# Performance work log

Measured on AMD Instinct MI355X. Metric: run time of the kernel, lower is better.

## Reference

```python
import jax, jax.numpy as jnp
import numpy as np

N = 50000
E = 800000
IN_C = 64
OUT_C = 64
K = 2
GATE_C = IN_C + OUT_C
LAMBDA_MAX = 2.0


def _lap_norm(edge_index, edge_weight, n):
    # PyG ChebConv norm: sym Laplacian L = I - D^-1/2 A D^-1/2, scaled 2L/lmax - I.
    # With lambda_max=2 the diagonal term is (2/lmax)*1 - 1 = 0, so only the
    # off-diagonal weights -(2/lmax) * w_norm remain.
    row, col = edge_index[0], edge_index[1]
    deg = jax.ops.segment_sum(edge_weight, row, num_segments=n)
    dinv = jnp.where(deg > 0, jax.lax.rsqrt(jnp.where(deg > 0, deg, 1.0)), 0.0)
    lw = -(2.0 / LAMBDA_MAX) * edge_weight * dinv[row] * dinv[col]
    diag = jnp.full((n,), 2.0 / LAMBDA_MAX - 1.0, edge_weight.dtype)  # zeros for lmax=2
    return row, col, lw, diag


def _cheb_conv(x, row, col, lw, diag, Ws, b):
    # Ws: [K, C_in, C_out]; Tx_0 = x, Tx_1 = L_hat x, Tx_k = 2 L_hat Tx_{k-1} - Tx_{k-2}
    n = x.shape[0]

    def prop(h):  # L_hat @ h  via edge gather/scatter + diagonal
        msg = lw[:, None] * h[col]                      # [E, C]
        return jax.ops.segment_sum(msg, row, num_segments=n) + diag[:, None] * h

    Tx0 = x
    out = Tx0 @ Ws[0]
    Tx1 = prop(x)
    out = out + Tx1 @ Ws[1]
    for k in range(2, K):
        Tx2 = 2.0 * prop(Tx1) - Tx0
        out = out + Tx2 @ Ws[k]
        Tx0, Tx1 = Tx1, Tx2
    return out + b


def setup_inputs() -> dict:
    key = jax.random.key(0)
    ks = jax.random.split(key, 10)
    scale = 1.0 / np.sqrt(GATE_C)
    x = jax.random.normal(ks[0], (N, IN_C), jnp.float32)
    edge_index = jax.random.randint(ks[1], (2, E), 0, N, jnp.int64)
    edge_weight = jax.random.uniform(ks[2], (E,), jnp.float32)
    hidden_state = jax.random.normal(ks[3], (N, OUT_C), jnp.float32)
    Wz = jax.random.normal(ks[4], (K, GATE_C, OUT_C), jnp.float32) * scale
    Wr = jax.random.normal(ks[5], (K, GATE_C, OUT_C), jnp.float32) * scale
    Wh = jax.random.normal(ks[6], (K, GATE_C, OUT_C), jnp.float32) * scale
    bz = jnp.zeros((OUT_C,), jnp.float32)
    br = jnp.zeros((OUT_C,), jnp.float32)
    bh = jnp.zeros((OUT_C,), jnp.float32)
    return {"x": x, "edge_index": edge_index, "edge_weight": edge_weight,
            "hidden_state": hidden_state, "Wz": Wz, "bz": bz,
            "Wr": Wr, "br": br, "Wh": Wh, "bh": bh}


def reference(x, edge_index, edge_weight, hidden_state, Wz, bz, Wr, br, Wh, bh):
    n = x.shape[0]
    row, col, lw, diag = _lap_norm(edge_index, edge_weight, n)
    gate_input = jnp.concatenate([x, hidden_state], axis=-1)          # [N, GATE_C]
    z = jax.nn.sigmoid(_cheb_conv(gate_input, row, col, lw, diag, Wz, bz))
    r = jax.nn.sigmoid(_cheb_conv(gate_input, row, col, lw, diag, Wr, br))
    cand_in = jnp.concatenate([x, r * hidden_state], axis=-1)
    h_tilde = jnp.tanh(_cheb_conv(cand_in, row, col, lw, diag, Wh, bh))
    return (1.0 - z) * hidden_state + z * h_tilde
```

## Files before the change

kernel.cpp:

```cpp
#include <hip/hip_runtime.h>
#include <cstdint>

#define N_NODES 50000
#define N_EDGES 800000
#define C 64
#define SLOTS 64
#define B_N 120
#define NB 417
#define PCAP 2560
#define STG_BLOCKS 126
#define STG_CHUNK 6350

typedef __attribute__((ext_vector_type(8))) short bf16x8;
typedef __attribute__((ext_vector_type(4))) float f32x4;

static constexpr size_t OFF_GCUR = 0;
static constexpr size_t OFF_DINV = 512;
static constexpr size_t OFF_CNT  = 50688;
static constexpr size_t OFF_BZR  = 100864;
static constexpr size_t OFF_BH   = 117248;
static constexpr size_t OFF_CSR  = 125440;
static constexpr size_t OFF_XH   = OFF_CSR + (size_t)N_NODES * 64;
static constexpr size_t OFF_XB   = OFF_XH + (size_t)N_NODES * C;
static constexpr size_t OFF_HB   = OFF_XB + (size_t)N_NODES * C / 2;
static constexpr size_t OFF_PXB  = OFF_HB + (size_t)N_NODES * C / 2;
static constexpr size_t OFF_PHB  = OFF_PXB + (size_t)N_NODES * C / 2;
static constexpr size_t OFF_RHB  = OFF_PHB + (size_t)N_NODES * C / 2;
static constexpr size_t OFF_RHD  = OFF_RHB + (size_t)N_NODES * C / 2;
static constexpr size_t OFF_STG  = OFF_PXB;

__device__ __forceinline__ short f2bf(float f) {
    unsigned u = __float_as_uint(f);
    u += 0x7fffu + ((u >> 16) & 1u);
    return (short)(u >> 16);
}
__device__ __forceinline__ float bf_lo(unsigned v) { return __uint_as_float(v << 16); }
__device__ __forceinline__ float bf_hi(unsigned v) { return __uint_as_float(v & 0xffff0000u); }
__device__ __forceinline__ float bfu(unsigned short v) { return __uint_as_float((unsigned)v << 16); }
__device__ __forceinline__ float fast_sigmoid(float v) { return 1.f / (1.f + __expf(-v)); }
__device__ __forceinline__ float fast_tanh(float v) { return 1.f - 2.f / (__expf(2.f * v) + 1.f); }

__global__ __launch_bounds__(256) void zero_pack_kernel(
        int* __restrict__ gcur,
        const float* __restrict__ Wz, const float* __restrict__ Wr,
        const float* __restrict__ Wh,
        short* __restrict__ Bzr, short* __restrict__ Bh) {
    if (blockIdx.x == 24) {
        gcur[threadIdx.x] = 0;
        gcur[256 + threadIdx.x] = 0;
        return;
    }
    int gid = blockIdx.x * 256 + threadIdx.x;
    if (gid < 4096) {
        int ktct = gid >> 6, lane = gid & 63;
        int kt = ktct >> 3, ct = ktct & 7;
        int colg = ct * 16 + (lane & 15);
        int k0 = kt * 32 + (lane >> 4) * 8;
        const float* W = (colg < 64) ? Wz : Wr;
        int c = colg & 63;
        short v[8];
        #pragma unroll
        for (int j = 0; j < 8; ++j) {
            int k = k0 + j;
            v[j] = f2bf(W[(k >> 7) * (128 * 64) + (k & 127) * 64 + c]);
        }
        *(bf16x8*)(Bzr + (size_t)ktct * 512 + lane * 8) = *(bf16x8*)v;
    } else {
        int idx = gid - 4096;
        int ktct = idx >> 6, lane = idx & 63;
        int kt = ktct >> 2, ct = ktct & 3;
        int colg = ct * 16 + (lane & 15);
        int k0 = kt * 32 + (lane >> 4) * 8;
        short v[8];
        #pragma unroll
        for (int j = 0; j < 8; ++j) {
            int k = k0 + j;
            v[j] = f2bf(Wh[(k >> 7) * (128 * 64) + (k & 127) * 64 + colg]);
        }
        *(bf16x8*)(Bh + (size_t)ktct * 512 + lane * 8) = *(bf16x8*)v;
    }
}

__global__ __launch_bounds__(512) void stage_kernel(
        const int* __restrict__ row, const int* __restrict__ col,
        const float* __restrict__ w,
        int* __restrict__ gcur, uint2* __restrict__ stg) {
    __shared__ int lcnt[NB];
    __shared__ int lbase[NB];
    int tid = threadIdx.x;
    int e0 = blockIdx.x * STG_CHUNK;
    int e1 = min(e0 + STG_CHUNK, N_EDGES);
    for (int i = tid; i < NB; i += 512) lcnt[i] = 0;
    __syncthreads();
    for (int e = e0 + tid; e < e1; e += 512)
        atomicAdd(&lcnt[row[e] / B_N], 1);
    __syncthreads();
    for (int i = tid; i < NB; i += 512) {
        int c = lcnt[i];
        lbase[i] = c ? atomicAdd(&gcur[i], c) : 0;
        lcnt[i] = 0;
    }
    __syncthreads();
    for (int e = e0 + tid; e < e1; e += 512) {
        int r = row[e];
        int b = r / B_N;
        int off = atomicAdd(&lcnt[b], 1);
        int pos = lbase[b] + off;
        unsigned cw = ((unsigned)col[e] << 16) | (unsigned short)f2bf(w[e]);
        if (pos < PCAP)
            stg[(size_t)b * PCAP + pos] = make_uint2((unsigned)(r - b * B_N), cw);
    }
}

__global__ __launch_bounds__(256) void sort_kernel(
        const int* __restrict__ gcur, const uint2* __restrict__ stg,
        const float* __restrict__ x, const float* __restrict__ h,
        unsigned* __restrict__ csr, int* __restrict__ cnt, float* __restrict__ dinv,
        unsigned* __restrict__ xh,
        unsigned short* __restrict__ xb, unsigned short* __restrict__ hb) {
    __shared__ int lcnt[B_N];
    __shared__ int lbase[B_N];
    __shared__ float ldeg[B_N];
    __shared__ float ldv[B_N];
    __shared__ int scanb[128];
    __shared__ unsigned lbuf[PCAP];
    __shared__ unsigned char lnode[PCAP];
    int b = blockIdx.x, tid = threadIdx.x;
    int n0 = b * B_N;
    int m = min(gcur[b], PCAP);
    for (int i = tid; i < B_N; i += 256) { lcnt[i] = 0; ldeg[i] = 0.f; }
    __syncthreads();
    const uint2* s = stg + (size_t)b * PCAP;
    for (int i = tid; i < m; i += 256) {
        uint2 e = s[i];
        atomicAdd(&lcnt[e.x], 1);
        atomicAdd(&ldeg[e.x], bf_lo(e.y));
    }
    __syncthreads();
    if (tid < 128) scanb[tid] = (tid < B_N) ? lcnt[tid] : 0;
    __syncthreads();
    for (int d = 1; d < 128; d <<= 1) {
        int v = 0;
        if (tid < 128 && tid >= d) v = scanb[tid - d];
        __syncthreads();
        if (tid < 128) scanb[tid] += v;
        __syncthreads();
    }
    if (tid < B_N) { lbase[tid] = scanb[tid] - lcnt[tid]; lcnt[tid] = 0; }
    __syncthreads();
    for (int i = tid; i < m; i += 256) {
        uint2 e = s[i];
        int off = atomicAdd(&lcnt[e.x], 1);
        int p = lbase[e.x] + off;
        lbuf[p] = e.y;
        lnode[p] = (unsigned char)e.x;
    }
    __syncthreads();
    for (int i = tid; i < m; i += 256) {
        int nl = lnode[i];
        int pos = i - lbase[nl];
        csr[(size_t)(n0 + nl) * SLOTS + pos] = lbuf[i];
    }
    if (tid < B_N) {
        int node = n0 + tid;
        if (node < N_NODES) {
            cnt[node] = lcnt[tid];
            float d = ldeg[tid];
            float dv = (d > 0.f) ? rsqrtf(d) : 0.f;
            dinv[node] = dv;
            ldv[tid] = dv;
        } else ldv[tid] = 0.f;
    }
    __syncthreads();
    for (int i = tid; i < B_N * 16; i += 256) {
        int g = n0 * 16 + i;
        if (g >= N_NODES * 16) continue;
        float dv = ldv[i >> 4];
        float4 xv = ((const float4*)x)[g];
        float4 hv = ((const float4*)h)[g];
        uint4 o;
        o.x = ((unsigned)(unsigned short)f2bf(hv.x * dv) << 16) | (unsigned short)f2bf(xv.x * dv);
        o.y = ((unsigned)(unsigned short)f2bf(hv.y * dv) << 16) | (unsigned short)f2bf(xv.y * dv);
        o.z = ((unsigned)(unsigned short)f2bf(hv.z * dv) << 16) | (unsigned short)f2bf(xv.z * dv);
        o.w = ((unsigned)(unsigned short)f2bf(hv.w * dv) << 16) | (unsigned short)f2bf(xv.w * dv);
        ((uint4*)xh)[g] = o;
        ((short4*)xb)[g] = make_short4(f2bf(xv.x), f2bf(xv.y), f2bf(xv.z), f2bf(xv.w));
        ((short4*)hb)[g] = make_short4(f2bf(hv.x), f2bf(hv.y), f2bf(hv.z), f2bf(hv.w));
    }
}

__global__ __launch_bounds__(256) void prop2_gather_kernel(
        const int* __restrict__ cnt, const unsigned* __restrict__ csr,
        const float* __restrict__ dinv, const unsigned* __restrict__ xh,
        unsigned short* __restrict__ Pxb, unsigned short* __restrict__ Phb) {
    int n = (blockIdx.x * 256 + threadIdx.x) >> 6;
    int lane = threadIdx.x & 63;
    if (n >= N_NODES) return;
    int m = min(cnt[n], SLOTS);
    const unsigned* s = csr + (size_t)n * SLOTS;
    float ax = 0.f, ah = 0.f;
    int e = 0;
    for (; e + 4 <= m; e += 4) {
        unsigned p0 = s[e], p1 = s[e + 1], p2 = s[e + 2], p3 = s[e + 3];
        unsigned v0 = xh[(p0 >> 16) * C + lane];
        unsigned v1 = xh[(p1 >> 16) * C + lane];
        unsigned v2 = xh[(p2 >> 16) * C + lane];
        unsigned v3 = xh[(p3 >> 16) * C + lane];
        float w0 = bf_lo(p0), w1 = bf_lo(p1), w2 = bf_lo(p2), w3 = bf_lo(p3);
        ax = fmaf(w0, bf_lo(v0), ax);  ah = fmaf(w0, bf_hi(v0), ah);
        ax = fmaf(w1, bf_lo(v1), ax);  ah = fmaf(w1, bf_hi(v1), ah);
        ax = fmaf(w2, bf_lo(v2), ax);  ah = fmaf(w2, bf_hi(v2), ah);
        ax = fmaf(w3, bf_lo(v3), ax);  ah = fmaf(w3, bf_hi(v3), ah);
    }
    for (; e < m; ++e) {
        unsigned p = s[e];
        unsigned v = xh[(p >> 16) * C + lane];
        float wv = bf_lo(p);
        ax = fmaf(wv, bf_lo(v), ax);
        ah = fmaf(wv, bf_hi(v), ah);
    }
    float sc = -dinv[n];
    Pxb[(size_t)n * C + lane] = (unsigned short)f2bf(sc * ax);
    Phb[(size_t)n * C + lane] = (unsigned short)f2bf(sc * ah);
}

__global__ __launch_bounds__(256) void prop1_gather_kernel(
        const int* __restrict__ cnt, const unsigned* __restrict__ csr,
        const float* __restrict__ dinv,
        const unsigned short* __restrict__ rhd, unsigned short* __restrict__ Prhb) {
    int n = (blockIdx.x * 256 + threadIdx.x) >> 6;
    int lane = threadIdx.x & 63;
    if (n >= N_NODES) return;
    int m = min(cnt[n], SLOTS);
    const unsigned* s = csr + (size_t)n * SLOTS;
    float acc = 0.f;
    int e = 0;
    for (; e + 4 <= m; e += 4) {
        unsigned p0 = s[e], p1 = s[e + 1], p2 = s[e + 2], p3 = s[e + 3];
        float v0 = bfu(rhd[(p0 >> 16) * C + lane]);
        float v1 = bfu(rhd[(p1 >> 16) * C + lane]);
        float v2 = bfu(rhd[(p2 >> 16) * C + lane]);
        float v3 = bfu(rhd[(p3 >> 16) * C + lane]);
        acc = fmaf(bf_lo(p0), v0, acc);
        acc = fmaf(bf_lo(p1), v1, acc);
        acc = fmaf(bf_lo(p2), v2, acc);
        acc = fmaf(bf_lo(p3), v3, acc);
    }
    for (; e < m; ++e) {
        unsigned p = s[e];
        acc = fmaf(bf_lo(p), bfu(rhd[(p >> 16) * C + lane]), acc);
    }
    Prhb[(size_t)n * C + lane] = (unsigned short)f2bf(-dinv[n] * acc);
}

__global__ __launch_bounds__(256) void gemm_zr_mfma_kernel(
        const unsigned short* __restrict__ xb, const unsigned short* __restrict__ hb,
        const unsigned short* __restrict__ Pxb, const unsigned short* __restrict__ Phb,
        const short* __restrict__ Bzr,
        const float* __restrict__ bz, const float* __restrict__ br,
        const float* __restrict__ dinv,
        float* __restrict__ z, unsigned short* __restrict__ rhb,
        unsigned short* __restrict__ rhd) {
    int wave = (blockIdx.x * 256 + threadIdx.x) >> 6;
    int lane = threadIdx.x & 63;
    int node0 = wave * 16;
    if (node0 >= N_NODES) return;
    int q = lane >> 4;
    int nodeA = node0 + (lane & 15);

    f32x4 acc[8];
    #pragma unroll
    for (int i = 0; i < 8; ++i) acc[i] = (f32x4){0.f, 0.f, 0.f, 0.f};

    const bf16x8* Bp = (const bf16x8*)Bzr;
    #pragma unroll
    for (int kt = 0; kt < 8; ++kt) {
        const unsigned short* src = (kt < 2) ? xb : (kt < 4) ? hb : (kt < 6) ? Pxb : Phb;
        bf16x8 a = *(const bf16x8*)(src + (size_t)nodeA * C + (kt & 1) * 32 + q * 8);
        #pragma unroll
        for (int ct = 0; ct < 8; ++ct) {
            bf16x8 bfr = Bp[(kt * 8 + ct) * 64 + lane];
            acc[ct] = __builtin_amdgcn_mfma_f32_16x16x32_bf16(a, bfr, acc[ct], 0, 0, 0);
        }
    }

    float dv[4];
    #pragma unroll
    for (int r = 0; r < 4; ++r) dv[r] = dinv[node0 + q * 4 + r];

    #pragma unroll
    for (int ct = 0; ct < 8; ++ct) {
        int colg = ct * 16 + (lane & 15);
        if (ct < 4) {
            float bias = bz[colg];
            #pragma unroll
            for (int r = 0; r < 4; ++r) {
                int node = node0 + q * 4 + r;
                z[(size_t)node * C + colg] = fast_sigmoid(acc[ct][r] + bias);
            }
        } else {
            int oc = colg - 64;
            float bias = br[oc];
            #pragma unroll
            for (int r = 0; r < 4; ++r) {
                int node = node0 + q * 4 + r;
                float sg = fast_sigmoid(acc[ct][r] + bias);
                float rhv = sg * bfu(hb[(size_t)node * C + oc]);
                rhb[(size_t)node * C + oc] = (unsigned short)f2bf(rhv);
                rhd[(size_t)node * C + oc] = (unsigned short)f2bf(rhv * dv[r]);
            }
        }
    }
}

__global__ __launch_bounds__(256) void gemm_h_mfma_kernel(
        const unsigned short* __restrict__ xb, const unsigned short* __restrict__ rhb,
        const unsigned short* __restrict__ Pxb, const unsigned short* __restrict__ Prhb,
        const short* __restrict__ Bh, const float* __restrict__ bh,
        const float* __restrict__ z,  const float* __restrict__ h,
        float* __restrict__ out) {
    int wave = (blockIdx.x * 256 + threadIdx.x) >> 6;
    int lane = threadIdx.x & 63;
    int node0 = wave * 16;
    if (node0 >= N_NODES) return;
    int q = lane >> 4;
    int nodeA = node0 + (lane & 15);

    f32x4 acc[4];
    #pragma unroll
    for (int i = 0; i < 4; ++i) acc[i] = (f32x4){0.f, 0.f, 0.f, 0.f};

    const bf16x8* Bp = (const bf16x8*)Bh;
    #pragma unroll
    for (int kt = 0; kt < 8; ++kt) {
        const unsigned short* src = (kt < 2) ? xb : (kt < 4) ? rhb : (kt < 6) ? Pxb : Prhb;
        bf16x8 a = *(const bf16x8*)(src + (size_t)nodeA * C + (kt & 1) * 32 + q * 8);
        #pragma unroll
        for (int ct = 0; ct < 4; ++ct) {
            bf16x8 bfr = Bp[(kt * 4 + ct) * 64 + lane];
            acc[ct] = __builtin_amdgcn_mfma_f32_16x16x32_bf16(a, bfr, acc[ct], 0, 0, 0);
        }
    }

    #pragma unroll
    for (int ct = 0; ct < 4; ++ct) {
        int oc = ct * 16 + (lane & 15);
        float bias = bh[oc];
        #pragma unroll
        for (int r = 0; r < 4; ++r) {
            int node = node0 + q * 4 + r;
            float ht = fast_tanh(acc[ct][r] + bias);
            float zz = z[(size_t)node * C + oc];
            float hv = h[(size_t)node * C + oc];
            out[(size_t)node * C + oc] = (1.f - zz) * hv + zz * ht;
        }
    }
}

extern "C" void kernel_launch(void* const* d_in, const int* in_sizes, int n_in,
                              void* d_out, int out_size, void* d_ws, size_t ws_size,
                              hipStream_t stream) {
    const float* x    = (const float*)d_in[0];
    const int*   eidx = (const int*)  d_in[1];
    const float* w    = (const float*)d_in[2];
    const float* h    = (const float*)d_in[3];
    const float* Wz   = (const float*)d_in[4];
    const float* bz   = (const float*)d_in[5];
    const float* Wr   = (const float*)d_in[6];
    const float* br   = (const float*)d_in[7];
    const float* Wh   = (const float*)d_in[8];
    const float* bh   = (const float*)d_in[9];
    float* out = (float*)d_out;
    float* ws  = (float*)d_ws;

    const int* row = eidx;
    const int* col = eidx + N_EDGES;

    int*            gcur = (int*)(ws + OFF_GCUR);
    float*          dinv = ws + OFF_DINV;
    int*            cnt  = (int*)(ws + OFF_CNT);
    unsigned*       csr  = (unsigned*)(ws + OFF_CSR);
    short*          Bzr  = (short*)(ws + OFF_BZR);
    short*          Bh   = (short*)(ws + OFF_BH);
    unsigned*       xh   = (unsigned*)(ws + OFF_XH);
    unsigned short* xb   = (unsigned short*)(ws + OFF_XB);
    unsigned short* hb   = (unsigned short*)(ws + OFF_HB);
    unsigned short* Pxb  = (unsigned short*)(ws + OFF_PXB);
    unsigned short* Phb  = (unsigned short*)(ws + OFF_PHB);
    unsigned short* rhb  = (unsigned short*)(ws + OFF_RHB);
    unsigned short* rhd  = (unsigned short*)(ws + OFF_RHD);
    uint2*          stg  = (uint2*)(ws + OFF_STG);
    float*          z    = out;

    zero_pack_kernel<<<25, 256, 0, stream>>>(gcur, Wz, Wr, Wh, Bzr, Bh);

    stage_kernel<<<STG_BLOCKS, 512, 0, stream>>>(row, col, w, gcur, stg);

    sort_kernel<<<NB, 256, 0, stream>>>(gcur, stg, x, h, csr, cnt, dinv, xh, xb, hb);

    prop2_gather_kernel<<<(N_NODES * 64 + 255) / 256, 256, 0, stream>>>(
        cnt, csr, dinv, xh, Pxb, Phb);

    {
        int waves = (N_NODES + 15) / 16;
        int blocks = (waves + 3) / 4;
        gemm_zr_mfma_kernel<<<blocks, 256, 0, stream>>>(
            xb, hb, Pxb, Phb, Bzr, bz, br, dinv, z, rhb, rhd);
    }

    prop1_gather_kernel<<<(N_NODES * 64 + 255) / 256, 256, 0, stream>>>(
        cnt, csr, dinv, rhd, Phb);

    {
        int waves = (N_NODES + 15) / 16;
        int blocks = (waves + 3) / 4;
        gemm_h_mfma_kernel<<<blocks, 256, 0, stream>>>(
            xb, rhb, Pxb, Phb, Bh, bh, z, h, out);
    }
}
```

Before: 228.5 us.

## Fuse sparse gather propagation into MFMA gate GEMM kernels via shared memory

Merges each gather-based Laplacian propagation kernel with the MFMA GEMM that consumes it. Each 256-thread block now handles 16 nodes: its waves gather propagated rows into LDS, synchronise, then split the output column tiles among themselves. This drops two kernel launches and the global round trip of Phb/Prhb, at the cost of fewer waves per node tile during the GEMM and a block-level barrier between gather and GEMM. Pxb is still written to global memory because the h-gate kernel needs it.

```diff
diff --git a/kernel.cpp b/kernel.cpp
--- a/kernel.cpp
+++ b/kernel.cpp
@@ -189,122 +189,104 @@
     }
 }
 
-__global__ __launch_bounds__(256) void prop2_gather_kernel(
+__global__ __launch_bounds__(256) void prop_gemm_zr_kernel(
         const int* __restrict__ cnt, const unsigned* __restrict__ csr,
         const float* __restrict__ dinv, const unsigned* __restrict__ xh,
-        unsigned short* __restrict__ Pxb, unsigned short* __restrict__ Phb) {
-    int n = (blockIdx.x * 256 + threadIdx.x) >> 6;
-    int lane = threadIdx.x & 63;
-    if (n >= N_NODES) return;
-    int m = min(cnt[n], SLOTS);
-    const unsigned* s = csr + (size_t)n * SLOTS;
-    float ax = 0.f, ah = 0.f;
-    int e = 0;
-    for (; e + 4 <= m; e += 4) {
-        unsigned p0 = s[e], p1 = s[e + 1], p2 = s[e + 2], p3 = s[e + 3];
-        unsigned v0 = xh[(p0 >> 16) * C + lane];
-        unsigned v1 = xh[(p1 >> 16) * C + lane];
-        unsigned v2 = xh[(p2 >> 16) * C + lane];
-        unsigned v3 = xh[(p3 >> 16) * C + lane];
-        float w0 = bf_lo(p0), w1 = bf_lo(p1), w2 = bf_lo(p2), w3 = bf_lo(p3);
-        ax = fmaf(w0, bf_lo(v0), ax);  ah = fmaf(w0, bf_hi(v0), ah);
-        ax = fmaf(w1, bf_lo(v1), ax);  ah = fmaf(w1, bf_hi(v1), ah);
-        ax = fmaf(w2, bf_lo(v2), ax);  ah = fmaf(w2, bf_hi(v2), ah);
-        ax = fmaf(w3, bf_lo(v3), ax);  ah = fmaf(w3, bf_hi(v3), ah);
-    }
-    for (; e < m; ++e) {
-        unsigned p = s[e];
-        unsigned v = xh[(p >> 16) * C + lane];
-        float wv = bf_lo(p);
-        ax = fmaf(wv, bf_lo(v), ax);
-        ah = fmaf(wv, bf_hi(v), ah);
-    }
-    float sc = -dinv[n];
-    Pxb[(size_t)n * C + lane] = (unsigned short)f2bf(sc * ax);
-    Phb[(size_t)n * C + lane] = (unsigned short)f2bf(sc * ah);
-}
-
-__global__ __launch_bounds__(256) void prop1_gather_kernel(
-        const int* __restrict__ cnt, const unsigned* __restrict__ csr,
-        const float* __restrict__ dinv,
-        const unsigned short* __restrict__ rhd, unsigned short* __restrict__ Prhb) {
-    int n = (blockIdx.x * 256 + threadIdx.x) >> 6;
-    int lane = threadIdx.x & 63;
-    if (n >= N_NODES) return;
-    int m = min(cnt[n], SLOTS);
-    const unsigned* s = csr + (size_t)n * SLOTS;
-    float acc = 0.f;
-    int e = 0;
-    for (; e + 4 <= m; e += 4) {
-        unsigned p0 = s[e], p1 = s[e + 1], p2 = s[e + 2], p3 = s[e + 3];
-        float v0 = bfu(rhd[(p0 >> 16) * C + lane]);
-        float v1 = bfu(rhd[(p1 >> 16) * C + lane]);
-        float v2 = bfu(rhd[(p2 >> 16) * C + lane]);
-        float v3 = bfu(rhd[(p3 >> 16) * C + lane]);
-        acc = fmaf(bf_lo(p0), v0, acc);
-        acc = fmaf(bf_lo(p1), v1, acc);
-        acc = fmaf(bf_lo(p2), v2, acc);
-        acc = fmaf(bf_lo(p3), v3, acc);
-    }
-    for (; e < m; ++e) {
-        unsigned p = s[e];
-        acc = fmaf(bf_lo(p), bfu(rhd[(p >> 16) * C + lane]), acc);
-    }
-    Prhb[(size_t)n * C + lane] = (unsigned short)f2bf(-dinv[n] * acc);
-}
-
-__global__ __launch_bounds__(256) void gemm_zr_mfma_kernel(
         const unsigned short* __restrict__ xb, const unsigned short* __restrict__ hb,
-        const unsigned short* __restrict__ Pxb, const unsigned short* __restrict__ Phb,
         const short* __restrict__ Bzr,
         const float* __restrict__ bz, const float* __restrict__ br,
-        const float* __restrict__ dinv,
+        unsigned short* __restrict__ Pxb,
         float* __restrict__ z, unsigned short* __restrict__ rhb,
         unsigned short* __restrict__ rhd) {
-    int wave = (blockIdx.x * 256 + threadIdx.x) >> 6;
-    int lane = threadIdx.x & 63;
-    int node0 = wave * 16;
-    if (node0 >= N_NODES) return;
+    __shared__ __align__(16) unsigned short lpx[16][72];
+    __shared__ __align__(16) unsigned short lph[16][72];
+    int tid = threadIdx.x;
+    int wid = tid >> 6, lane = tid & 63;
+    int node0 = blockIdx.x * 16;
+
+    #pragma unroll
+    for (int i = 0; i < 4; ++i) {
+        int nl = wid * 4 + i;
+        int n = node0 + nl;
+        int m = min(cnt[n], SLOTS);
+        const unsigned* s = csr + (size_t)n * SLOTS;
+        float ax = 0.f, ah = 0.f;
+        int e = 0;
+        for (; e + 4 <= m; e += 4) {
+            unsigned p0 = s[e], p1 = s[e + 1], p2 = s[e + 2], p3 = s[e + 3];
+            unsigned v0 = xh[(p0 >> 16) * C + lane];
+            unsigned v1 = xh[(p1 >> 16) * C + lane];
+            unsigned v2 = xh[(p2 >> 16) * C + lane];
+            unsigned v3 = xh[(p3 >> 16) * C + lane];
+            float w0 = bf_lo(p0), w1 = bf_lo(p1), w2 = bf_lo(p2), w3 = bf_lo(p3);
+            ax = fmaf(w0, bf_lo(v0), ax);  ah = fmaf(w0, bf_hi(v0), ah);
+            ax = fmaf(w1, bf_lo(v1), ax);  ah = fmaf(w1, bf_hi(v1), ah);
+            ax = fmaf(w2, bf_lo(v2), ax);  ah = fmaf(w2, bf_hi(v2), ah);
+            ax = fmaf(w3, bf_lo(v3), ax);  ah = fmaf(w3, bf_hi(v3), ah);
+        }
+        for (; e < m; ++e) {
+            unsigned p = s[e];
+            unsigned v = xh[(p >> 16) * C + lane];
+            float wv = bf_lo(p);
+            ax = fmaf(wv, bf_lo(v), ax);
+            ah = fmaf(wv, bf_hi(v), ah);
+        }
+        float sc = -dinv[n];
+        unsigned short px = (unsigned short)f2bf(sc * ax);
+        unsigned short ph = (unsigned short)f2bf(sc * ah);
+        lpx[nl][lane] = px;
+        lph[nl][lane] = ph;
+        Pxb[(size_t)n * C + lane] = px;
+    }
+    __syncthreads();
+
     int q = lane >> 4;
-    int nodeA = node0 + (lane & 15);
-
-    f32x4 acc[8];
-    #pragma unroll
-    for (int i = 0; i < 8; ++i) acc[i] = (f32x4){0.f, 0.f, 0.f, 0.f};
-
+    int nl = lane & 15;
+    f32x4 acc[2];
+    acc[0] = (f32x4){0.f, 0.f, 0.f, 0.f};
+    acc[1] = (f32x4){0.f, 0.f, 0.f, 0.f};
     const bf16x8* Bp = (const bf16x8*)Bzr;
     #pragma unroll
     for (int kt = 0; kt < 8; ++kt) {
-        const unsigned short* src = (kt < 2) ? xb : (kt < 4) ? hb : (kt < 6) ? Pxb : Phb;
-        bf16x8 a = *(const bf16x8*)(src + (size_t)nodeA * C + (kt & 1) * 32 + q * 8);
-        #pragma unroll
-        for (int ct = 0; ct < 8; ++ct) {
+        bf16x8 a;
+        if (kt < 4) {
+            const unsigned short* src = (kt < 2) ? xb : hb;
+            a = *(const bf16x8*)(src + (size_t)(node0 + nl) * C + (kt & 1) * 32 + q * 8);
+        } else {
+            const unsigned short* src = (kt < 6) ? &lpx[0][0] : &lph[0][0];
+            a = *(const bf16x8*)(src + nl * 72 + (kt & 1) * 32 + q * 8);
+        }
+        #pragma unroll
+        for (int c2 = 0; c2 < 2; ++c2) {
+            int ct = wid * 2 + c2;
             bf16x8 bfr = Bp[(kt * 8 + ct) * 64 + lane];
-            acc[ct] = __builtin_amdgcn_mfma_f32_16x16x32_bf16(a, bfr, acc[ct], 0, 0, 0);
-        }
-    }
-
-    float dv[4];
-    #pragma unroll
-    for (int r = 0; r < 4; ++r) dv[r] = dinv[node0 + q * 4 + r];
-
-    #pragma unroll
-    for (int ct = 0; ct < 8; ++ct) {
-        int colg = ct * 16 + (lane & 15);
-        if (ct < 4) {
+            acc[c2] = __builtin_amdgcn_mfma_f32_16x16x32_bf16(a, bfr, acc[c2], 0, 0, 0);
+        }
+    }
+
+    if (wid < 2) {
+        #pragma unroll
+        for (int c2 = 0; c2 < 2; ++c2) {
+            int colg = (wid * 2 + c2) * 16 + nl;
             float bias = bz[colg];
             #pragma unroll
             for (int r = 0; r < 4; ++r) {
                 int node = node0 + q * 4 + r;
-                z[(size_t)node * C + colg] = fast_sigmoid(acc[ct][r] + bias);
+                z[(size_t)node * C + colg] = fast_sigmoid(acc[c2][r] + bias);
             }
-        } else {
-            int oc = colg - 64;
+        }
+    } else {
+        float dv[4];
+        #pragma unroll
+        for (int r = 0; r < 4; ++r) dv[r] = dinv[node0 + q * 4 + r];
+        #pragma unroll
+        for (int c2 = 0; c2 < 2; ++c2) {
+            int oc = (wid * 2 + c2 - 4) * 16 + nl;
             float bias = br[oc];
             #pragma unroll
             for (int r = 0; r < 4; ++r) {
                 int node = node0 + q * 4 + r;
-                float sg = fast_sigmoid(acc[ct][r] + bias);
+                float sg = fast_sigmoid(acc[c2][r] + bias);
                 float rhv = sg * bfu(hb[(size_t)node * C + oc]);
                 rhb[(size_t)node * C + oc] = (unsigned short)f2bf(rhv);
                 rhd[(size_t)node * C + oc] = (unsigned short)f2bf(rhv * dv[r]);
@@ -313,47 +295,72 @@
     }
 }
 
-__global__ __launch_bounds__(256) void gemm_h_mfma_kernel(
+__global__ __launch_bounds__(256) void prop_gemm_h_kernel(
+        const int* __restrict__ cnt, const unsigned* __restrict__ csr,
+        const float* __restrict__ dinv, const unsigned short* __restrict__ rhd,
         const unsigned short* __restrict__ xb, const unsigned short* __restrict__ rhb,
-        const unsigned short* __restrict__ Pxb, const unsigned short* __restrict__ Prhb,
+        const unsigned short* __restrict__ Pxb,
         const short* __restrict__ Bh, const float* __restrict__ bh,
-        const float* __restrict__ z,  const float* __restrict__ h,
+        const float* __restrict__ z, const float* __restrict__ h,
         float* __restrict__ out) {
-    int wave = (blockIdx.x * 256 + threadIdx.x) >> 6;
-    int lane = threadIdx.x & 63;
-    int node0 = wave * 16;
-    if (node0 >= N_NODES) return;
+    __shared__ __align__(16) unsigned short lpr[16][72];
+    int tid = threadIdx.x;
+    int wid = tid >> 6, lane = tid & 63;
+    int node0 = blockIdx.x * 16;
+
+    #pragma unroll
+    for (int i = 0; i < 4; ++i) {
+        int nl = wid * 4 + i;
+        int n = node0 + nl;
+        int m = min(cnt[n], SLOTS);
+        const unsigned* s = csr + (size_t)n * SLOTS;
+        float acc = 0.f;
+        int e = 0;
+        for (; e + 4 <= m; e += 4) {
+            unsigned p0 = s[e], p1 = s[e + 1], p2 = s[e + 2], p3 = s[e + 3];
+            float v0 = bfu(rhd[(p0 >> 16) * C + lane]);
+            float v1 = bfu(rhd[(p1 >> 16) * C + lane]);
+            float v2 = bfu(rhd[(p2 >> 16) * C + lane]);
+            float v3 = bfu(rhd[(p3 >> 16) * C + lane]);
+            acc = fmaf(bf_lo(p0), v0, acc);
+            acc = fmaf(bf_lo(p1), v1, acc);
+            acc = fmaf(bf_lo(p2), v2, acc);
+            acc = fmaf(bf_lo(p3), v3, acc);
+        }
+        for (; e < m; ++e) {
+            unsigned p = s[e];
+            acc = fmaf(bf_lo(p), bfu(rhd[(p >> 16) * C + lane]), acc);
+        }
+        lpr[nl][lane] = (unsigned short)f2bf(-dinv[n] * acc);
+    }
+    __syncthreads();
+
     int q = lane >> 4;
-    int nodeA = node0 + (lane & 15);
-
-    f32x4 acc[4];
-    #pragma unroll
-    for (int i = 0; i < 4; ++i) acc[i] = (f32x4){0.f, 0.f, 0.f, 0.f};
-
+    int nl = lane & 15;
+    f32x4 acc = (f32x4){0.f, 0.f, 0.f, 0.f};
     const bf16x8* Bp = (const bf16x8*)Bh;
     #pragma unroll
     for (int kt = 0; kt < 8; ++kt) {
-        const unsigned short* src = (kt < 2) ? xb : (kt < 4) ? rhb : (kt < 6) ? Pxb : Prhb;
-        bf16x8 a = *(const bf16x8*)(src + (size_t)nodeA * C + (kt & 1) * 32 + q * 8);
-        #pragma unroll
-        for (int ct = 0; ct < 4; ++ct) {
-            bf16x8 bfr = Bp[(kt * 4 + ct) * 64 + lane];
-            acc[ct] = __builtin_amdgcn_mfma_f32_16x16x32_bf16(a, bfr, acc[ct], 0, 0, 0);
-        }
-    }
-
+        bf16x8 a;
+        if (kt < 6) {
+            const unsigned short* src = (kt < 2) ? xb : (kt < 4) ? rhb : Pxb;
+            a = *(const bf16x8*)(src + (size_t)(node0 + nl) * C + (kt & 1) * 32 + q * 8);
+        } else {
+            a = *(const bf16x8*)(&lpr[0][0] + nl * 72 + (kt & 1) * 32 + q * 8);
+        }
+        bf16x8 bfr = Bp[(kt * 4 + wid) * 64 + lane];
+        acc = __builtin_amdgcn_mfma_f32_16x16x32_bf16(a, bfr, acc, 0, 0, 0);
+    }
+
+    int oc = wid * 16 + nl;
+    float bias = bh[oc];
     #pragma unroll
-    for (int ct = 0; ct < 4; ++ct) {
-        int oc = ct * 16 + (lane & 15);
-        float bias = bh[oc];
-        #pragma unroll
-        for (int r = 0; r < 4; ++r) {
-            int node = node0 + q * 4 + r;
-            float ht = fast_tanh(acc[ct][r] + bias);
-            float zz = z[(size_t)node * C + oc];
-            float hv = h[(size_t)node * C + oc];
-            out[(size_t)node * C + oc] = (1.f - zz) * hv + zz * ht;
-        }
+    for (int r = 0; r < 4; ++r) {
+        int node = node0 + q * 4 + r;
+        float ht = fast_tanh(acc[r] + bias);
+        float zz = z[(size_t)node * C + oc];
+        float hv = h[(size_t)node * C + oc];
+        out[(size_t)node * C + oc] = (1.f - zz) * hv + zz * ht;
     }
 }
 
@@ -386,7 +393,6 @@
     unsigned short* xb   = (unsigned short*)(ws + OFF_XB);
     unsigned short* hb   = (unsigned short*)(ws + OFF_HB);
     unsigned short* Pxb  = (unsigned short*)(ws + OFF_PXB);
-    unsigned short* Phb  = (unsigned short*)(ws + OFF_PHB);
     unsigned short* rhb  = (unsigned short*)(ws + OFF_RHB);
     unsigned short* rhd  = (unsigned short*)(ws + OFF_RHD);
     uint2*          stg  = (uint2*)(ws + OFF_STG);
@@ -398,23 +404,9 @@
 
     sort_kernel<<<NB, 256, 0, stream>>>(gcur, stg, x, h, csr, cnt, dinv, xh, xb, hb);
 
-    prop2_gather_kernel<<<(N_NODES * 64 + 255) / 256, 256, 0, stream>>>(
-        cnt, csr, dinv, xh, Pxb, Phb);
-
-    {
-        int waves = (N_NODES + 15) / 16;
-        int blocks = (waves + 3) / 4;
-        gemm_zr_mfma_kernel<<<blocks, 256, 0, stream>>>(
-            xb, hb, Pxb, Phb, Bzr, bz, br, dinv, z, rhb, rhd);
-    }
-
-    prop1_gather_kernel<<<(N_NODES * 64 + 255) / 256, 256, 0, stream>>>(
-        cnt, csr, dinv, rhd, Phb);
-
-    {
-        int waves = (N_NODES + 15) / 16;
-        int blocks = (waves + 3) / 4;
-        gemm_h_mfma_kernel<<<blocks, 256, 0, stream>>>(
-            xb, rhb, Pxb, Phb, Bh, bh, z, h, out);
-    }
-}
+    prop_gemm_zr_kernel<<<N_NODES / 16, 256, 0, stream>>>(
+        cnt, csr, dinv, xh, xb, hb, Bzr, bz, br, Pxb, z, rhb, rhd);
+
+    prop_gemm_h_kernel<<<N_NODES / 16, 256, 0, stream>>>(
+        cnt, csr, dinv, rhd, xb, rhb, Pxb, Bh, bh, z, h, out);
+}
```

Result: no change. 228.8 us (+0.1%).
